# Performance work log

Measured on AMD Instinct MI355X. Metric: run time of the kernel, lower is better.

Reference implementation:

```python
import jax, jax.numpy as jnp
import numpy as np

D_MODEL = 1024
HEAD_SIZE = 64
B, T = 4, 4096


def setup_inputs() -> dict:
    key = jax.random.key(0)
    k1, k2, k3, k4, k5, k6 = jax.random.split(key, 6)
    q = jax.random.normal(k1, (B, T, D_MODEL), dtype=jnp.float32)
    k = jax.random.normal(k2, (B, T, D_MODEL), dtype=jnp.float32)
    v = jax.random.normal(k3, (B, T, D_MODEL), dtype=jnp.float32)
    # bias-free Linear weights stored as [d_model, head_size] so proj = x @ W
    s = 1.0 / np.sqrt(D_MODEL)
    Wq = jax.random.uniform(k4, (D_MODEL, HEAD_SIZE), jnp.float32, -s, s)
    Wk = jax.random.uniform(k5, (D_MODEL, HEAD_SIZE), jnp.float32, -s, s)
    Wv = jax.random.uniform(k6, (D_MODEL, HEAD_SIZE), jnp.float32, -s, s)
    # [T,T] bool mask, True = keep (lower-triangular, exercises masking path)
    attn_mask = jnp.tril(jnp.ones((T, T), dtype=jnp.bool_))
    return {"q": q, "k": k, "v": v, "Wq": Wq, "Wk": Wk, "Wv": Wv,
            "attn_mask": attn_mask}


def reference(q, k, v, Wq, Wk, Wv, attn_mask):
    # projections: [B,T,d_model] @ [d_model,head] -> [B,T,head]
    qh = q @ Wq
    kh = k @ Wk
    vh = v @ Wv
    # raw scores [B,T,T]; attention_operation is Identity
    att = jnp.einsum('bqh,bkh->bqk', qh, kh)
    # mask BEFORE scaling (matches original; -inf/scale == -inf)
    att = jnp.where(attn_mask[None, :, :], att, -jnp.inf)
    scale = jnp.asarray(HEAD_SIZE ** 0.5, att.dtype)
    probs = jax.nn.softmax(att / scale, axis=-1)
    # dropout rate is 0.0 -> no-op
    return jnp.einsum('bqk,bkh->bqh', probs, vh)
```

## Files before the change

kernel.cpp:

```cpp
#include <hip/hip_runtime.h>
#include <hip/hip_fp16.h>

typedef _Float16 f16;
typedef __fp16 h16x2 __attribute__((ext_vector_type(2)));
typedef _Float16 f16x8 __attribute__((ext_vector_type(8)));
typedef _Float16 f16x4v __attribute__((ext_vector_type(4)));
typedef float f32x4 __attribute__((ext_vector_type(4)));
typedef float f32x16 __attribute__((ext_vector_type(16)));
typedef unsigned int u32;
typedef u32 u32x4 __attribute__((ext_vector_type(4)));

constexpr int DM = 1024;
constexpr int HS = 64;
constexpr int NBATCH = 4;
constexpr int T = 4096;
constexpr float CEXP = 0.18033688011112042f;

#if __has_builtin(__builtin_amdgcn_exp2f)
#define EXP2(x) __builtin_amdgcn_exp2f(x)
#else
#define EXP2(x) exp2f(x)
#endif

static __device__ __forceinline__ u32 pack2_f16(float a, float b) {
  union { f16 h[2]; u32 u; } cv;
  cv.h[0] = (f16)a; cv.h[1] = (f16)b;
  return cv.u;
}

static __device__ __forceinline__ f16x8 cvt8(const f32x4& a0, const f32x4& a1) {
  union { h16x2 p[4]; f16x8 v; } cv;
  cv.p[0] = __builtin_amdgcn_cvt_pkrtz(a0[0], a0[1]);
  cv.p[1] = __builtin_amdgcn_cvt_pkrtz(a0[2], a0[3]);
  cv.p[2] = __builtin_amdgcn_cvt_pkrtz(a1[0], a1[1]);
  cv.p[3] = __builtin_amdgcn_cvt_pkrtz(a1[2], a1[3]);
  return cv.v;
}

static __device__ __forceinline__ void gload_lds16(const void* g, void* l) {
  __builtin_amdgcn_global_load_lds(
      (__attribute__((address_space(1))) void*)(g),
      (__attribute__((address_space(3))) void*)(l), 16, 0, 0);
}

__global__ void wtrans_kernel(const float* __restrict__ Wq, const float* __restrict__ Wk,
                              const float* __restrict__ Wv, f16* __restrict__ WTf) {
  const int which = blockIdx.y;
  const float* __restrict__ W = (which == 0) ? Wq : ((which == 1) ? Wk : Wv);
  const int o8 = blockIdx.x * 256 + threadIdx.x;
  const int t = o8 >> 8;
  const int cb = (o8 >> 6) & 3;
  const int g = (o8 >> 4) & 3;
  const int q15 = o8 & 15;
  const int col = cb * 16 + q15;
  f16x8 v;
#pragma unroll
  for (int e = 0; e < 8; ++e) v[e] = (f16)W[(t * 32 + 8 * g + e) * 64 + col];
  *(f16x8*)(WTf + which * 65536 + o8 * 8) = v;
}

__global__ __launch_bounds__(512, 4) void proj_kernel(
    const float* __restrict__ xq, const float* __restrict__ xk, const float* __restrict__ xv,
    const f16* __restrict__ WTf, f16* __restrict__ qh, f16* __restrict__ kh,
    f16* __restrict__ vhT) {
  __shared__ __align__(16) char As[8][8192];

  const int which = blockIdx.y;
  const float* __restrict__ x = (which == 0) ? xq : ((which == 1) ? xk : xv);
  const int tid = threadIdx.x;
  const int lane = tid & 63, w = tid >> 6;
  const int q15 = lane & 15, g = lane >> 4;
  const int row0 = blockIdx.x * 16;
  const char* __restrict__ xbase = (const char*)x;

  const int l7 = lane & 7, l3 = lane >> 3;
  const int swz = ((l7 ^ l3) * 16);
#pragma unroll
  for (int t = 0; t < 4; ++t)
#pragma unroll
    for (int j = 0; j < 2; ++j) {
      const int r = 8 * j + l3;
      gload_lds16(xbase + (size_t)(row0 + r) * 4096 + (size_t)(w * 128 + t * 32) * 4 + swz,
                  &As[w][t * 2048 + j * 1024]);
    }

  const char* __restrict__ wfb = (const char*)(WTf + which * 65536) + lane * 16;
  f16x8 B[16];
#pragma unroll
  for (int i = 0; i < 16; ++i)
    B[i] = *(const f16x8*)(wfb + (size_t)(w * 16 + i) * 1024);

  asm volatile("s_waitcnt vmcnt(0)" ::: "memory");
  __builtin_amdgcn_sched_barrier(0);

  f32x4 acc[4];
#pragma unroll
  for (int cb = 0; cb < 4; ++cb) acc[cb] = (f32x4){0.f, 0.f, 0.f, 0.f};

  const char* pa = &As[w][0] + q15 * 128;
  const int rx = (q15 & 7) * 16;
#pragma unroll
  for (int t = 0; t < 4; ++t) {
    const f32x4 a0 = *(const f32x4*)(pa + t * 2048 + (((2 * g + 0) * 16) ^ rx));
    const f32x4 a1 = *(const f32x4*)(pa + t * 2048 + (((2 * g + 1) * 16) ^ rx));
    const f16x8 af = cvt8(a0, a1);
#pragma unroll
    for (int cb = 0; cb < 4; ++cb)
      acc[cb] = __builtin_amdgcn_mfma_f32_16x16x32_f16(af, B[t * 4 + cb], acc[cb], 0, 0, 0);
  }

  float* part = (float*)&As[w][0];
#pragma unroll
  for (int cb = 0; cb < 4; ++cb)
#pragma unroll
    for (int j = 0; j < 4; ++j)
      part[(4 * g + j) * 68 + cb * 16 + q15] = acc[cb][j];
  __syncthreads();

  const int col = tid & 63;
  const int rp = (tid >> 6) * 2;
  float v0 = 0.f, v1 = 0.f;
#pragma unroll
  for (int w2 = 0; w2 < 8; ++w2) {
    const float* p2 = (const float*)&As[w2][0];
    v0 += p2[rp * 68 + col];
    v1 += p2[(rp + 1) * 68 + col];
  }

  if (which < 2) {
    f16* __restrict__ outp = (which == 0) ? qh : kh;
    outp[(size_t)(row0 + rp) * HS + col] = (f16)v0;
    outp[(size_t)(row0 + rp + 1) * HS + col] = (f16)v1;
  } else {
    const int b = row0 >> 12;
    const int trow = (row0 & (T - 1)) + rp;
    *(u32*)(vhT + (size_t)b * HS * T + (size_t)col * T + trow) = pack2_f16(v0, v1);
  }
}

__global__ __launch_bounds__(512, 4) void attn_kernel(
    const f16* __restrict__ qh, const f16* __restrict__ kh,
    const f16* __restrict__ vhT, float* __restrict__ out) {
  __shared__ float sO[4][64][33];
  __shared__ float sMm[8][32];
  __shared__ float sLs[8][32];

  const int tid = threadIdx.x;
  const int lane = tid & 63, w = tid >> 6;
  const int q31 = lane & 31, hi = lane >> 5;

  const int id = blockIdx.x;
  const int b = (id & 7) >> 1;
  const int qt = 127 - 2 * (id >> 3) - (id & 1);
  const int q0 = qt * 32;

  const f16* __restrict__ kbase = kh + (size_t)b * T * HS;
  const f16* __restrict__ vbase = vhT + (size_t)b * HS * T;
  const f16* __restrict__ qp = qh + (size_t)(b * T + q0 + q31) * HS + 8 * hi;

  f16x8 qb[4];
#pragma unroll
  for (int kt = 0; kt < 4; ++kt) qb[kt] = *(const f16x8*)(qp + 16 * kt);

  f32x16 o0, o1;
#pragma unroll
  for (int i = 0; i < 16; ++i) { o0[i] = 0.f; o1[i] = 0.f; }
  float m = -1e30f, lsum = 0.f;

  const int nblk = qt + 1;
  for (int blk = w; blk < nblk; blk += 8) {
    const int kv0 = blk * 32;
    const f16* kr = kbase + (size_t)(kv0 + q31) * HS + 8 * hi;
    f16x8 ka0 = *(const f16x8*)(kr);
    f16x8 ka1 = *(const f16x8*)(kr + 16);
    f16x8 ka2 = *(const f16x8*)(kr + 32);
    f16x8 ka3 = *(const f16x8*)(kr + 48);

    f32x16 s;
#pragma unroll
    for (int i = 0; i < 16; ++i) s[i] = 0.f;
    s = __builtin_amdgcn_mfma_f32_32x32x16_f16(ka0, qb[0], s, 0, 0, 0);
    s = __builtin_amdgcn_mfma_f32_32x32x16_f16(ka1, qb[1], s, 0, 0, 0);
    s = __builtin_amdgcn_mfma_f32_32x32x16_f16(ka2, qb[2], s, 0, 0, 0);
    s = __builtin_amdgcn_mfma_f32_32x32x16_f16(ka3, qb[3], s, 0, 0, 0);

    const f16* vr = vbase + (size_t)q31 * T + kv0 + 8 * hi;
    f16x8 v00 = *(const f16x8*)(vr);
    f16x8 v01 = *(const f16x8*)(vr + 16);
    f16x8 v10 = *(const f16x8*)(vr + (size_t)32 * T);
    f16x8 v11 = *(const f16x8*)(vr + (size_t)32 * T + 16);

    if (blk == qt) {
#pragma unroll
      for (int r = 0; r < 16; ++r) {
        const int kl = (r & 3) + 8 * (r >> 2) + 4 * hi;
        if (kl > q31) s[r] = -1e30f;
      }
    }

    float pm = s[0];
#pragma unroll
    for (int r = 1; r < 16; ++r) pm = fmaxf(pm, s[r]);
    pm = fmaxf(pm, __shfl_xor(pm, 32));
    if (!__all(pm <= m + 32.f)) {
      const float mn = fmaxf(m, pm);
      const float r = EXP2((m - mn) * CEXP);
      lsum *= r;
#pragma unroll
      for (int i = 0; i < 16; ++i) { o0[i] *= r; o1[i] *= r; }
      m = mn;
    }

    float p[16];
    float ps = 0.f;
#pragma unroll
    for (int r = 0; r < 16; ++r) { p[r] = EXP2((s[r] - m) * CEXP); ps += p[r]; }
    ps += __shfl_xor(ps, 32);
    lsum += ps;

    u32 c[8], xg[8];
#pragma unroll
    for (int i = 0; i < 8; ++i) c[i] = pack2_f16(p[2 * i], p[2 * i + 1]);
#pragma unroll
    for (int i = 0; i < 8; ++i) xg[i] = (u32)__shfl_xor((int)c[i], 32);
    union { u32x4 u; f16x8 f; } f1, f2;
    f1.u = (u32x4){ hi ? xg[2] : c[0], hi ? xg[3] : c[1], hi ? c[2] : xg[0], hi ? c[3] : xg[1] };
    f2.u = (u32x4){ hi ? xg[6] : c[4], hi ? xg[7] : c[5], hi ? c[6] : xg[4], hi ? c[7] : xg[5] };

    o0 = __builtin_amdgcn_mfma_f32_32x32x16_f16(v00, f1.f, o0, 0, 0, 0);
    o0 = __builtin_amdgcn_mfma_f32_32x32x16_f16(v01, f2.f, o0, 0, 0, 0);
    o1 = __builtin_amdgcn_mfma_f32_32x32x16_f16(v10, f1.f, o1, 0, 0, 0);
    o1 = __builtin_amdgcn_mfma_f32_32x32x16_f16(v11, f2.f, o1, 0, 0, 0);
  }

  if (lane < 32) sMm[w][q31] = m;
  __syncthreads();
  float M = sMm[0][q31];
#pragma unroll
  for (int w2 = 1; w2 < 8; ++w2) M = fmaxf(M, sMm[w2][q31]);
  const float sc = EXP2((m - M) * CEXP);
  if (lane < 32) sLs[w][q31] = lsum * sc;
#pragma unroll
  for (int i = 0; i < 16; ++i) { o0[i] *= sc; o1[i] *= sc; }

  if (w >= 4) {
#pragma unroll
    for (int r = 0; r < 16; ++r) {
      const int d = (r & 3) + 8 * (r >> 2) + 4 * hi;
      sO[w - 4][d][q31] = o0[r];
      sO[w - 4][d + 32][q31] = o1[r];
    }
  }
  __syncthreads();
  if (w < 4) {
#pragma unroll
    for (int r = 0; r < 16; ++r) {
      const int d = (r & 3) + 8 * (r >> 2) + 4 * hi;
      sO[w][d][q31] += o0[r];
      sO[w][d + 32][q31] += o1[r];
    }
  }
  __syncthreads();

  const int q = tid >> 4;
  const int d0 = (tid & 15) * 4;
  float L = 0.f;
#pragma unroll
  for (int w2 = 0; w2 < 8; ++w2) L += sLs[w2][q];
  const float invL = 1.f / L;
  float4 rv;
  rv.x = (sO[0][d0 + 0][q] + sO[1][d0 + 0][q] + sO[2][d0 + 0][q] + sO[3][d0 + 0][q]) * invL;
  rv.y = (sO[0][d0 + 1][q] + sO[1][d0 + 1][q] + sO[2][d0 + 1][q] + sO[3][d0 + 1][q]) * invL;
  rv.z = (sO[0][d0 + 2][q] + sO[1][d0 + 2][q] + sO[2][d0 + 2][q] + sO[3][d0 + 2][q]) * invL;
  rv.w = (sO[0][d0 + 3][q] + sO[1][d0 + 3][q] + sO[2][d0 + 3][q] + sO[3][d0 + 3][q]) * invL;
  *(float4*)(out + (size_t)(b * T + q0 + q) * HS + d0) = rv;
}

extern "C" void kernel_launch(void* const* d_in, const int* in_sizes, int n_in,
                              void* d_out, int out_size, void* d_ws, size_t ws_size,
                              hipStream_t stream) {
  const float* q  = (const float*)d_in[0];
  const float* k  = (const float*)d_in[1];
  const float* v  = (const float*)d_in[2];
  const float* Wq = (const float*)d_in[3];
  const float* Wk = (const float*)d_in[4];
  const float* Wv = (const float*)d_in[5];
  float* out = (float*)d_out;

  f16* qh  = (f16*)d_ws;
  f16* kh  = qh  + (size_t)NBATCH * T * HS;
  f16* vhT = kh  + (size_t)NBATCH * T * HS;
  f16* WTf = vhT + (size_t)NBATCH * T * HS;

  wtrans_kernel<<<dim3(32, 3), 256, 0, stream>>>(Wq, Wk, Wv, WTf);
  proj_kernel<<<dim3(NBATCH * T / 16, 3), 512, 0, stream>>>(q, k, v, WTf, qh, kh, vhT);
  attn_kernel<<<dim3(T / 32 * NBATCH), 512, 0, stream>>>(qh, kh, vhT, out);
}
```

Before: 96.75 us.

## Restructure projection: stage full weight in LDS, per-wave full-K loop with pipelined loads

The projection kernel now copies the entire 128KB f16 weight slice into LDS once per block. Each of 4 waves computes a 16-row tile over the full K=1024 dimension, streaming activations with a 4-deep software-pipelined run of inline-asm global loads and explicit vmcnt waits. This removes the old split-K design, its cross-wave LDS reduction and its per-block register load of weights, and cuts the grid from 1024x3 blocks to 256x3. The cost is a large LDS footprint that limits occupancy to one block per CU, plus more LDS traffic for B operands.

```diff
diff --git a/kernel.cpp b/kernel.cpp
--- a/kernel.cpp
+++ b/kernel.cpp
@@ -59,82 +59,90 @@
   *(f16x8*)(WTf + which * 65536 + o8 * 8) = v;
 }
 
-__global__ __launch_bounds__(512, 4) void proj_kernel(
+__global__ __launch_bounds__(256) void proj_kernel(
     const float* __restrict__ xq, const float* __restrict__ xk, const float* __restrict__ xv,
     const f16* __restrict__ WTf, f16* __restrict__ qh, f16* __restrict__ kh,
     f16* __restrict__ vhT) {
-  __shared__ __align__(16) char As[8][8192];
+  __shared__ __align__(16) char Bs[131072];
 
   const int which = blockIdx.y;
   const float* __restrict__ x = (which == 0) ? xq : ((which == 1) ? xk : xv);
   const int tid = threadIdx.x;
   const int lane = tid & 63, w = tid >> 6;
   const int q15 = lane & 15, g = lane >> 4;
-  const int row0 = blockIdx.x * 16;
-  const char* __restrict__ xbase = (const char*)x;
-
-  const int l7 = lane & 7, l3 = lane >> 3;
-  const int swz = ((l7 ^ l3) * 16);
-#pragma unroll
-  for (int t = 0; t < 4; ++t)
-#pragma unroll
-    for (int j = 0; j < 2; ++j) {
-      const int r = 8 * j + l3;
-      gload_lds16(xbase + (size_t)(row0 + r) * 4096 + (size_t)(w * 128 + t * 32) * 4 + swz,
-                  &As[w][t * 2048 + j * 1024]);
-    }
-
-  const char* __restrict__ wfb = (const char*)(WTf + which * 65536) + lane * 16;
-  f16x8 B[16];
-#pragma unroll
-  for (int i = 0; i < 16; ++i)
-    B[i] = *(const f16x8*)(wfb + (size_t)(w * 16 + i) * 1024);
-
-  asm volatile("s_waitcnt vmcnt(0)" ::: "memory");
+  const int row0 = blockIdx.x * 64 + w * 16;
+
+  const char* __restrict__ wsrc = (const char*)(WTf + (size_t)which * 65536);
+#pragma unroll
+  for (int j = 0; j < 32; ++j)
+    gload_lds16(wsrc + j * 4096 + w * 1024 + (lane & 63) * 16,
+                &Bs[j * 4096 + w * 1024]);
   __builtin_amdgcn_sched_barrier(0);
 
+  const size_t aaddr =
+      (size_t)((const char*)x + (size_t)(row0 + q15) * 4096 + 32 * g);
+  f32x4 ld[16][4];
+#define AISSUE(s)                                                                       \
+  {                                                                                     \
+    const size_t ab = aaddr + (size_t)((s) * 256);                                      \
+    asm volatile("global_load_dwordx4 %0, %1, off"            : "=v"(ld[s][0]) : "v"(ab)); \
+    asm volatile("global_load_dwordx4 %0, %1, off offset:16"  : "=v"(ld[s][1]) : "v"(ab)); \
+    asm volatile("global_load_dwordx4 %0, %1, off offset:128" : "=v"(ld[s][2]) : "v"(ab)); \
+    asm volatile("global_load_dwordx4 %0, %1, off offset:144" : "=v"(ld[s][3]) : "v"(ab)); \
+  }
+  AISSUE(0) AISSUE(1) AISSUE(2) AISSUE(3)
+
+  asm volatile("s_waitcnt vmcnt(16)" ::: "memory");
+  __builtin_amdgcn_sched_barrier(0);
+  __builtin_amdgcn_s_barrier();
+  __builtin_amdgcn_sched_barrier(0);
+
   f32x4 acc[4];
 #pragma unroll
   for (int cb = 0; cb < 4; ++cb) acc[cb] = (f32x4){0.f, 0.f, 0.f, 0.f};
 
-  const char* pa = &As[w][0] + q15 * 128;
-  const int rx = (q15 & 7) * 16;
-#pragma unroll
-  for (int t = 0; t < 4; ++t) {
-    const f32x4 a0 = *(const f32x4*)(pa + t * 2048 + (((2 * g + 0) * 16) ^ rx));
-    const f32x4 a1 = *(const f32x4*)(pa + t * 2048 + (((2 * g + 1) * 16) ^ rx));
-    const f16x8 af = cvt8(a0, a1);
-#pragma unroll
-    for (int cb = 0; cb < 4; ++cb)
-      acc[cb] = __builtin_amdgcn_mfma_f32_16x16x32_f16(af, B[t * 4 + cb], acc[cb], 0, 0, 0);
-  }
-
-  float* part = (float*)&As[w][0];
-#pragma unroll
-  for (int cb = 0; cb < 4; ++cb)
-#pragma unroll
-    for (int j = 0; j < 4; ++j)
-      part[(4 * g + j) * 68 + cb * 16 + q15] = acc[cb][j];
-  __syncthreads();
-
-  const int col = tid & 63;
-  const int rp = (tid >> 6) * 2;
-  float v0 = 0.f, v1 = 0.f;
-#pragma unroll
-  for (int w2 = 0; w2 < 8; ++w2) {
-    const float* p2 = (const float*)&As[w2][0];
-    v0 += p2[rp * 68 + col];
-    v1 += p2[(rp + 1) * 68 + col];
-  }
+#pragma unroll
+  for (int s = 0; s < 16; ++s) {
+    if (s < 13)      asm volatile("s_waitcnt vmcnt(12)" ::: "memory");
+    else if (s == 13) asm volatile("s_waitcnt vmcnt(8)" ::: "memory");
+    else if (s == 14) asm volatile("s_waitcnt vmcnt(4)" ::: "memory");
+    else              asm volatile("s_waitcnt vmcnt(0)" ::: "memory");
+    __builtin_amdgcn_sched_barrier(0);
+    if (s + 4 < 16) AISSUE(s + 4)
+
+    const f16x8 af0 = cvt8(ld[s][0], ld[s][1]);
+    const f16x8 af1 = cvt8(ld[s][2], ld[s][3]);
+    const char* bb = &Bs[0] + s * 8192 + lane * 16;
+#pragma unroll
+    for (int cb = 0; cb < 4; ++cb) {
+      const f16x8 b0 = *(const f16x8*)(bb + cb * 1024);
+      acc[cb] = __builtin_amdgcn_mfma_f32_16x16x32_f16(af0, b0, acc[cb], 0, 0, 0);
+    }
+#pragma unroll
+    for (int cb = 0; cb < 4; ++cb) {
+      const f16x8 b1 = *(const f16x8*)(bb + 4096 + cb * 1024);
+      acc[cb] = __builtin_amdgcn_mfma_f32_16x16x32_f16(af1, b1, acc[cb], 0, 0, 0);
+    }
+  }
+#undef AISSUE
 
   if (which < 2) {
     f16* __restrict__ outp = (which == 0) ? qh : kh;
-    outp[(size_t)(row0 + rp) * HS + col] = (f16)v0;
-    outp[(size_t)(row0 + rp + 1) * HS + col] = (f16)v1;
+#pragma unroll
+    for (int cb = 0; cb < 4; ++cb)
+#pragma unroll
+      for (int j = 0; j < 4; ++j)
+        outp[(size_t)(row0 + 4 * g + j) * HS + cb * 16 + q15] = (f16)acc[cb][j];
   } else {
     const int b = row0 >> 12;
-    const int trow = (row0 & (T - 1)) + rp;
-    *(u32*)(vhT + (size_t)b * HS * T + (size_t)col * T + trow) = pack2_f16(v0, v1);
+    const int t0 = (row0 & (T - 1)) + 4 * g;
+#pragma unroll
+    for (int cb = 0; cb < 4; ++cb) {
+      f16x4v pv;
+#pragma unroll
+      for (int j = 0; j < 4; ++j) pv[j] = (f16)acc[cb][j];
+      *(f16x4v*)(vhT + (size_t)b * HS * T + (size_t)(cb * 16 + q15) * T + t0) = pv;
+    }
   }
 }
 
@@ -293,6 +301,6 @@
   f16* WTf = vhT + (size_t)NBATCH * T * HS;
 
   wtrans_kernel<<<dim3(32, 3), 256, 0, stream>>>(Wq, Wk, Wv, WTf);
-  proj_kernel<<<dim3(NBATCH * T / 16, 3), 512, 0, stream>>>(q, k, v, WTf, qh, kh, vhT);
+  proj_kernel<<<dim3(256, 3), 256, 0, stream>>>(q, k, v, WTf, qh, kh, vhT);
   attn_kernel<<<dim3(T / 32 * NBATCH), 512, 0, stream>>>(qh, kh, vhT, out);
 }
```

Result: faster. 91.19 us (-5.7%).
